# Kernel optimization log

Hardware: AMD Instinct MI355X
Metric: run time of the kernel (lower is better)

The kernel has to match this reference:

```python
import jax, jax.numpy as jnp
import numpy as np

LN_EPS = 1e-3  # keras LayerNormalization default epsilon
LEAKY_SLOPE = 0.2  # tf 'leaky_relu' default alpha


def layer_norm(x, gamma, beta):
    mu = jnp.mean(x, axis=-1, keepdims=True)
    var = jnp.mean(jnp.square(x - mu), axis=-1, keepdims=True)
    return (x - mu) * jax.lax.rsqrt(var + LN_EPS) * gamma + beta


def attention_head(q_in, kv_in, Wk, Wv, Wq, causal):
    # q_in: [b, sq, d], kv_in: [b, sk, d]
    K = jnp.einsum('bsd,de->bse', kv_in, Wk)
    V = jnp.einsum('bsd,de->bse', kv_in, Wv)
    Q = jnp.einsum('bsd,de->bse', q_in, Wq)
    sk = K.shape[1]
    # NOTE: original scales by sqrt(window_size_keys), i.e. key seq length
    scores = jnp.einsum('bqe,bke->bqk', Q, K) / jnp.sqrt(jnp.float32(sk))
    if causal:
        sq = Q.shape[1]
        mask = jnp.triu(jnp.full((sq, sk), -jnp.inf, dtype=scores.dtype), k=1)
        scores = scores + mask
    probs = jax.nn.softmax(scores, axis=-1)
    return jnp.einsum('bqk,bke->bqe', probs, V)


def setup_inputs() -> dict:
    key = jax.random.key(0)
    ks = jax.random.split(key, 12)
    B, S, D, H = 4, 4096, 256, 400
    p = lambda k, shp: jax.random.normal(k, shp, dtype=jnp.float32) * 0.1
    return {
        'inputs': jax.random.normal(ks[0], (B, S, D), dtype=jnp.float32),
        'context_sequence': jax.random.normal(ks[1], (B, S, D), dtype=jnp.float32),
        'sa_Wk': p(ks[2], (D, D)),
        'sa_Wv': p(ks[3], (D, D)),
        'sa_Wq': p(ks[4], (D, D)),
        'ca_Wk': p(ks[5], (D, D)),
        'ca_Wv': p(ks[6], (D, D)),
        'ca_Wq': p(ks[7], (D, D)),
        'W1': p(ks[8], (D, H)),
        'b1': jnp.zeros((H,), dtype=jnp.float32),
        'W2': p(ks[9], (H, D)),
        'b2': jnp.zeros((D,), dtype=jnp.float32),
        'gamma': jnp.ones((D,), dtype=jnp.float32),
        'beta': jnp.zeros((D,), dtype=jnp.float32),
    }


def reference(inputs, context_sequence, sa_Wk, sa_Wv, sa_Wq, ca_Wk, ca_Wv, ca_Wq,
              W1, b1, W2, b2, gamma, beta):
    # 1) masked self-attention + residual + LN (shared LN params)
    in_attn = attention_head(inputs, inputs, sa_Wk, sa_Wv, sa_Wq, causal=True)
    x = layer_norm(in_attn + inputs, gamma, beta)
    # 2) unmasked cross-attention (queries = x, keys/values = context) + residual + LN
    ctx_attn = attention_head(x, context_sequence, ca_Wk, ca_Wv, ca_Wq, causal=False)
    y = layer_norm(ctx_attn + x, gamma, beta)
    # 3) FFN (Dense 400 leaky_relu -> Dense emb) + residual + LN
    h = jax.nn.leaky_relu(jnp.einsum('bsd,dh->bsh', y, W1) + b1, negative_slope=LEAKY_SLOPE)
    ff = jnp.einsum('bsh,hd->bsd', h, W2) + b2
    return layer_norm(ff + y, gamma, beta)
```

## Files before the change

kernel.cpp:

```cpp
#include <hip/hip_runtime.h>

typedef __bf16  bf16x4 __attribute__((ext_vector_type(4)));
typedef __bf16  bf16x8 __attribute__((ext_vector_type(8)));
typedef float   f32x4  __attribute__((ext_vector_type(4)));
typedef unsigned int u32;

constexpr int BM = 128, BN = 128, BK = 32;

__device__ __forceinline__ void async_cp16(const __bf16* g, __bf16* lds) {
    __builtin_amdgcn_global_load_lds(
        (const __attribute__((address_space(1))) u32*)g,
        (__attribute__((address_space(3))) u32*)lds, 16, 0, 0);
}

__device__ __forceinline__ int swz(int row, int q) {
    return row * BK + (((q + (row >> 1)) & 3) << 3);
}

template<int EPI>
__launch_bounds__(256)
__global__ void gemm_nt(const __bf16* __restrict__ Aall, const __bf16* __restrict__ Ball,
                        const float* __restrict__ bias,
                        void* __restrict__ C0, void* __restrict__ C1, void* __restrict__ C2,
                        int N, int K, long ldb, long sA, long sB, long sC,
                        int nTx, int klen, long pstrideB)
{
    const int bx = blockIdx.x;
    const int chunk = bx / nTx;
    const int n0 = (bx - chunk * nTx) * BN;
    const int m0 = blockIdx.y * BM;
    const int bz = blockIdx.z;
    const int kbase = chunk * klen;

    const __bf16* A  = Aall + (long)bz * sA;
    const __bf16* Bt = Ball + (long)bz * sB;

    __shared__ alignas(16) __bf16 As[BM * BK];
    __shared__ alignas(16) __bf16 Bs[BN * BK];

    const int tid = threadIdx.x;
    const int wave = tid >> 6, lane = tid & 63;
    const int wm = (wave >> 1) * 64, wn = (wave & 1) * 64;
    const int quad = lane >> 4, l16 = lane & 15;

    const int row0 = tid >> 2, sl0 = tid & 3;
    const int ks0 = (sl0 - (row0 >> 1)) & 3;
    const int row1 = row0 + 64;
    const int ks1 = (sl0 - (row1 >> 1)) & 3;
    const __bf16* gA0 = A  + (long)(m0 + row0) * K + kbase + ks0 * 8;
    const __bf16* gA1 = A  + (long)(m0 + row1) * K + kbase + ks1 * 8;
    const __bf16* gB0 = Bt + (long)(n0 + row0) * ldb + kbase + ks0 * 8;
    const __bf16* gB1 = Bt + (long)(n0 + row1) * ldb + kbase + ks1 * 8;
    __bf16* ldsA0 = As + wave * 512;
    __bf16* ldsA1 = As + 2048 + wave * 512;
    __bf16* ldsB0 = Bs + wave * 512;
    __bf16* ldsB1 = Bs + 2048 + wave * 512;

    f32x4 acc[4][4];
    #pragma unroll
    for (int i = 0; i < 4; i++)
        #pragma unroll
        for (int j = 0; j < 4; j++) { f32x4 z = {0.f, 0.f, 0.f, 0.f}; acc[i][j] = z; }

    for (int kk = 0; kk < klen; kk += BK) {
        __syncthreads();
        async_cp16(gA0, ldsA0);
        async_cp16(gA1, ldsA1);
        async_cp16(gB0, ldsB0);
        async_cp16(gB1, ldsB1);
        gA0 += BK; gA1 += BK; gB0 += BK; gB1 += BK;
        __syncthreads();

        bf16x8 af[4], bg[4];
        #pragma unroll
        for (int i = 0; i < 4; i++) {
            af[i] = *(const bf16x8*)(As + swz(wm + i * 16 + l16, quad));
            bg[i] = *(const bf16x8*)(Bs + swz(wn + i * 16 + l16, quad));
        }
        #pragma unroll
        for (int i = 0; i < 4; i++)
            #pragma unroll
            for (int j = 0; j < 4; j++)
                acc[i][j] = __builtin_amdgcn_mfma_f32_16x16x32_bf16(af[i], bg[j], acc[i][j], 0, 0, 0);
    }

    char* cb = (char*)C0 + (EPI == 3 ? (long)chunk * pstrideB : 0);
    #pragma unroll
    for (int j = 0; j < 4; j++) {
        const int col = n0 + wn + j * 16 + l16;
        const float bv = (EPI == 2) ? bias[col] : 0.f;
        #pragma unroll
        for (int i = 0; i < 4; i++) {
            #pragma unroll
            for (int r = 0; r < 4; r++) {
                const int row = m0 + wm + i * 16 + quad * 4 + r;
                float c = acc[i][j][r];
                if (EPI == 2) { c += bv; c = c > 0.f ? c : 0.2f * c; }
                if (EPI == 1 || EPI == 3)
                    ((__bf16*)cb)[(long)bz * sC + (long)row * N + col] = (__bf16)c;
                else if (EPI == 2)
                    ((__bf16*)cb)[(long)row * N + col] = (__bf16)c;
                else {
                    const int seg = col >> 8;
                    __bf16* dst = seg == 0 ? (__bf16*)C0 : (seg == 1 ? (__bf16*)C1 : (__bf16*)C2);
                    dst[(long)row * 256 + (col & 255)] = (__bf16)c;
                }
            }
        }
    }
}

template<bool CAUSAL>
__launch_bounds__(256)
__global__ void scores_nt(const __bf16* __restrict__ Qall, const __bf16* __restrict__ Kall,
                          __bf16* __restrict__ SCall, float* __restrict__ side, float scale)
{
    constexpr int S = 4096, KD = 256;
    const int kt = blockIdx.x, mt = blockIdx.y;
    if (CAUSAL && kt > (mt | 1)) return;
    const int n0 = kt * 64, m0 = mt * 64;
    const int bz = blockIdx.z;
    const __bf16* Q  = Qall + (long)bz * S * KD;
    const __bf16* Kp = Kall + (long)bz * S * KD;

    __shared__ alignas(16) __bf16 As[64 * 64];
    __shared__ alignas(16) __bf16 Bs[64 * 64];

    const int tid = threadIdx.x;
    const int wave = tid >> 6, lane = tid & 63;
    const int quad = lane >> 4, l16 = lane & 15;
    const int wq = wave * 16;

    const int rowb = tid >> 3;
    const int gslot = (tid & 7) ^ (rowb & 7);
    const __bf16* gA0 = Q  + (long)(m0 + rowb) * KD + gslot * 8;
    const __bf16* gA1 = Q  + (long)(m0 + 32 + rowb) * KD + gslot * 8;
    const __bf16* gB0 = Kp + (long)(n0 + rowb) * KD + gslot * 8;
    const __bf16* gB1 = Kp + (long)(n0 + 32 + rowb) * KD + gslot * 8;
    const int wb = (tid & ~63) * 8;

    f32x4 acc[4];
    #pragma unroll
    for (int j = 0; j < 4; j++) { f32x4 z = {0.f, 0.f, 0.f, 0.f}; acc[j] = z; }

    for (int kk = 0; kk < KD; kk += 64) {
        __syncthreads();
        async_cp16(gA0 + kk, As + wb);
        async_cp16(gA1 + kk, As + 2048 + wb);
        async_cp16(gB0 + kk, Bs + wb);
        async_cp16(gB1 + kk, Bs + 2048 + wb);
        __syncthreads();
        #pragma unroll
        for (int t2 = 0; t2 < 2; t2++) {
            const int ra = wq + l16;
            bf16x8 af = *(const bf16x8*)(As + ra * 64 + (((t2 * 4 + quad) ^ (ra & 7)) << 3));
            #pragma unroll
            for (int j = 0; j < 4; j++) {
                const int rb = j * 16 + l16;
                bf16x8 bg = *(const bf16x8*)(Bs + rb * 64 + (((t2 * 4 + quad) ^ (rb & 7)) << 3));
                acc[j] = __builtin_amdgcn_mfma_f32_16x16x32_bf16(af, bg, acc[j], 0, 0, 0);
            }
        }
    }

    __bf16* sc = SCall + (long)bz * S * S;
    float se[4] = {0.f, 0.f, 0.f, 0.f};
    #pragma unroll
    for (int j = 0; j < 4; j++) {
        const int col = n0 + j * 16 + l16;
        #pragma unroll
        for (int r = 0; r < 4; r++) {
            const int row = m0 + wq + quad * 4 + r;
            float e = __expf(acc[j][r] * scale);
            if (CAUSAL && kt >= mt && col > row) e = 0.f;
            sc[(long)row * S + col] = (__bf16)e;
            se[r] += e;
        }
    }
    #pragma unroll
    for (int st = 1; st < 16; st <<= 1)
        #pragma unroll
        for (int r = 0; r < 4; r++) se[r] += __shfl_xor(se[r], st);
    if (l16 == 0) {
        float* sd = side + ((long)bz * 64 + kt) * 4096;
        #pragma unroll
        for (int r = 0; r < 4; r++) sd[m0 + wq + quad * 4 + r] = se[r];
    }
}

template<int CMODE>
__launch_bounds__(256)
__global__ void pv_nt(const __bf16* __restrict__ SCall, const __bf16* __restrict__ Vt,
                      __bf16* __restrict__ pbuf, int nsplit, long pstrideE)
{
    constexpr int S = 4096, D = 256, R = 16384;
    const int bx = blockIdx.x;
    const int lin = (bx >> 5) * 8 + (bx & 7);
    const int nt = (bx >> 3) & 3;
    const int per_b = 32 * nsplit;
    const int bz = lin / per_b;
    const int rem = lin - bz * per_b;
    const int chunk = rem >> 5;
    const int m0 = (rem & 31) * 128;
    const int n0 = nt * 64;
    int kbase, klocal;
    if (CMODE == 2) { const int kl = (m0 + 128) / nsplit; kbase = chunk * kl; klocal = kl; }
    else            { const int kl = S / nsplit;          kbase = chunk * kl; klocal = kl; }

    const __bf16* A = SCall + (long)bz * S * S;
    const __bf16* B = Vt + (long)bz * S;

    __shared__ alignas(16) __bf16 As[128 * 32];
    __shared__ alignas(16) __bf16 Bs[64 * 32];

    const int tid = threadIdx.x;
    const int wave = tid >> 6, lane = tid & 63;
    const int wm = (wave >> 1) * 64, wn2 = (wave & 1) * 32;
    const int quad = lane >> 4, l16 = lane & 15;

    const int row0 = tid >> 2, sl0 = tid & 3;
    const int ks0 = (sl0 - (row0 >> 1)) & 3;
    const int row1 = row0 + 64;
    const int ks1 = (sl0 - (row1 >> 1)) & 3;
    const __bf16* gA0 = A + (long)(m0 + row0) * S + kbase + ks0 * 8;
    const __bf16* gA1 = A + (long)(m0 + row1) * S + kbase + ks1 * 8;
    const __bf16* gB0 = B + (long)(n0 + row0) * R + kbase + ks0 * 8;
    __bf16* ldsA0 = As + wave * 512;
    __bf16* ldsA1 = As + 2048 + wave * 512;
    __bf16* ldsB0 = Bs + wave * 512;

    f32x4 acc[4][2];
    #pragma unroll
    for (int i = 0; i < 4; i++)
        #pragma unroll
        for (int j = 0; j < 2; j++) { f32x4 z = {0.f, 0.f, 0.f, 0.f}; acc[i][j] = z; }

    for (int kk = 0; kk < klocal; kk += 32) {
        __syncthreads();
        async_cp16(gA0, ldsA0);
        async_cp16(gA1, ldsA1);
        async_cp16(gB0, ldsB0);
        gA0 += 32; gA1 += 32; gB0 += 32;
        __syncthreads();

        bf16x8 af[4], bg[2];
        #pragma unroll
        for (int i = 0; i < 4; i++)
            af[i] = *(const bf16x8*)(As + swz(wm + i * 16 + l16, quad));
        #pragma unroll
        for (int j = 0; j < 2; j++)
            bg[j] = *(const bf16x8*)(Bs + swz(wn2 + j * 16 + l16, quad));
        #pragma unroll
        for (int i = 0; i < 4; i++)
            #pragma unroll
            for (int j = 0; j < 2; j++)
                acc[i][j] = __builtin_amdgcn_mfma_f32_16x16x32_bf16(af[i], bg[j], acc[i][j], 0, 0, 0);
    }

    __bf16* cb = pbuf + (long)chunk * pstrideE + (long)bz * S * D;
    #pragma unroll
    for (int j = 0; j < 2; j++) {
        const int col = n0 + wn2 + j * 16 + l16;
        #pragma unroll
        for (int i = 0; i < 4; i++)
            #pragma unroll
            for (int r = 0; r < 4; r++) {
                const int row = m0 + wm + i * 16 + quad * 4 + r;
                cb[(long)row * D + col] = (__bf16)acc[i][j][r];
            }
    }
}

template<bool CAUSAL>
__global__ void reduce_inv(const float* __restrict__ side, float* __restrict__ inv)
{
    const int i = blockIdx.x * 256 + threadIdx.x;
    const int b = i >> 12, r = i & 4095;
    const float* sp = side + (long)b * 64 * 4096 + r;
    const int lim = CAUSAL ? 2 * ((r >> 7) + 1) : 64;
    float s = 0.f;
    for (int t = 0; t < lim; t++) s += sp[(long)t * 4096];
    inv[i] = 1.f / s;
}

template<int NP>
__launch_bounds__(256)
__global__ void ln_res(const __bf16* __restrict__ p, long pstr,
                       const float* __restrict__ resid, const float* __restrict__ invs,
                       const float* __restrict__ bias,
                       const float* __restrict__ gamma, const float* __restrict__ beta,
                       float* __restrict__ outf, __bf16* __restrict__ outb)
{
    const int row  = blockIdx.x * 4 + (threadIdx.x >> 6);
    const int lane = threadIdx.x & 63;
    const long vi = (long)row * 64 + lane;
    float p0 = 0.f, p1 = 0.f, p2 = 0.f, p3 = 0.f;
    #pragma unroll
    for (int i = 0; i < NP; i++) {
        bf16x4 vp = ((const bf16x4*)(p + (long)i * pstr))[vi];
        p0 += (float)vp[0]; p1 += (float)vp[1]; p2 += (float)vp[2]; p3 += (float)vp[3];
    }
    if (invs) { const float iv = invs[row]; p0 *= iv; p1 *= iv; p2 *= iv; p3 *= iv; }
    float4 vr = ((const float4*)resid)[vi];
    float x0 = vr.x + p0, x1 = vr.y + p1, x2 = vr.z + p2, x3 = vr.w + p3;
    if (bias) {
        float4 vb = ((const float4*)bias)[lane];
        x0 += vb.x; x1 += vb.y; x2 += vb.z; x3 += vb.w;
    }
    float s = x0 + x1 + x2 + x3;
    #pragma unroll
    for (int off = 32; off; off >>= 1) s += __shfl_xor(s, off);
    const float mu = s * (1.f / 256.f);
    float d0 = x0 - mu, d1 = x1 - mu, d2 = x2 - mu, d3 = x3 - mu;
    float s2 = d0 * d0 + d1 * d1 + d2 * d2 + d3 * d3;
    #pragma unroll
    for (int off = 32; off; off >>= 1) s2 += __shfl_xor(s2, off);
    const float rs = rsqrtf(s2 * (1.f / 256.f) + 1e-3f);
    const float4 g  = ((const float4*)gamma)[lane];
    const float4 be = ((const float4*)beta)[lane];
    float o0 = d0 * rs * g.x + be.x, o1 = d1 * rs * g.y + be.y;
    float o2 = d2 * rs * g.z + be.z, o3 = d3 * rs * g.w + be.w;
    float4 o; o.x = o0; o.y = o1; o.z = o2; o.w = o3;
    ((float4*)outf)[vi] = o;
    if (outb) {
        bf16x4 ob; ob[0] = (__bf16)o0; ob[1] = (__bf16)o1; ob[2] = (__bf16)o2; ob[3] = (__bf16)o3;
        ((bf16x4*)outb)[vi] = ob;
    }
}

__device__ __forceinline__ void tp(const float* __restrict__ src, __bf16* __restrict__ dst,
                                   int rows, int cols, int rowsP, int i)
{
    const int c = i / rowsP, r = i - c * rowsP;
    const float v = (r < rows && c < cols) ? src[r * cols + c] : 0.f;
    dst[i] = (__bf16)v;
}

__global__ void prep_all(const float4* __restrict__ inA, const float4* __restrict__ inC,
                         bf16x4* __restrict__ outA, bf16x4* __restrict__ outC,
                         const float* __restrict__ sWq, const float* __restrict__ sWk,
                         const float* __restrict__ sWv,
                         const float* __restrict__ cWq, const float* __restrict__ cWk,
                         const float* __restrict__ cWv,
                         const float* __restrict__ W1, const float* __restrict__ W2,
                         __bf16* __restrict__ wqk_s, __bf16* __restrict__ wv_s,
                         __bf16* __restrict__ wq_c, __bf16* __restrict__ wk_c,
                         __bf16* __restrict__ wv_c,
                         __bf16* __restrict__ W1t, __bf16* __restrict__ W2t,
                         const float* __restrict__ b1, float* __restrict__ b1p)
{
    const int bx = blockIdx.x, tid = threadIdx.x;
    if (bx < 8192) {
        const bool a = bx < 4096;
        const long j = (long)(a ? bx : bx - 4096) * 256 + tid;
        float4 v = (a ? inA : inC)[j];
        bf16x4 o; o[0] = (__bf16)v.x; o[1] = (__bf16)v.y; o[2] = (__bf16)v.z; o[3] = (__bf16)v.w;
        (a ? outA : outC)[j] = o;
    }
    else if (bx < 8448)  tp(sWq, wqk_s,          256, 256, 256, (bx - 8192)  * 256 + tid);
    else if (bx < 8704)  tp(sWk, wqk_s + 65536,  256, 256, 256, (bx - 8448)  * 256 + tid);
    else if (bx < 8960)  tp(sWv, wv_s,           256, 256, 256, (bx - 8704)  * 256 + tid);
    else if (bx < 9216)  tp(cWq, wq_c,           256, 256, 256, (bx - 8960)  * 256 + tid);
    else if (bx < 9472)  tp(cWk, wk_c,           256, 256, 256, (bx - 9216)  * 256 + tid);
    else if (bx < 9728)  tp(cWv, wv_c,           256, 256, 256, (bx - 9472)  * 256 + tid);
    else if (bx < 10240) tp(W1,  W1t,            256, 400, 256, (bx - 9728)  * 256 + tid);
    else if (bx < 10752) tp(W2,  W2t,            400, 256, 512, (bx - 10240) * 256 + tid);
    else { const int i = (bx - 10752) * 256 + tid; if (i < 512) b1p[i] = (i < 400) ? b1[i] : 0.f; }
}

extern "C" void kernel_launch(void* const* d_in, const int* in_sizes, int n_in,
                              void* d_out, int out_size, void* d_ws, size_t ws_size,
                              hipStream_t stream)
{
    constexpr int B = 4, S = 4096, D = 256, H = 400, Hp = 512;
    constexpr int R = B * S;
    constexpr float SCALE = 1.f / 64.f;

    const float* inputs = (const float*)d_in[0];
    const float* ctx    = (const float*)d_in[1];
    const float* sa_Wk  = (const float*)d_in[2];
    const float* sa_Wv  = (const float*)d_in[3];
    const float* sa_Wq  = (const float*)d_in[4];
    const float* ca_Wk  = (const float*)d_in[5];
    const float* ca_Wv  = (const float*)d_in[6];
    const float* ca_Wq  = (const float*)d_in[7];
    const float* W1     = (const float*)d_in[8];
    const float* b1     = (const float*)d_in[9];
    const float* W2     = (const float*)d_in[10];
    const float* b2     = (const float*)d_in[11];
    const float* gamma  = (const float*)d_in[12];
    const float* beta   = (const float*)d_in[13];
    float* out = (float*)d_out;

    char* ws = (char*)d_ws;
    size_t off = 0;
    auto alloc = [&](size_t bytes) -> char* {
        char* p = ws + off; off += (bytes + 255) & ~size_t(255); return p;
    };
    __bf16* bfA  = (__bf16*)alloc((size_t)R * D * 2);
    __bf16* bfC  = (__bf16*)alloc((size_t)R * D * 2);
    __bf16* Qb   = (__bf16*)alloc((size_t)R * D * 2);
    __bf16* Kb   = (__bf16*)alloc((size_t)R * D * 2);
    __bf16* Vt   = (__bf16*)alloc((size_t)D * R * 2);
    __bf16* h    = (__bf16*)alloc((size_t)R * Hp * 2);
    float*  x    = (float*)alloc((size_t)R * D * 4);
    float*  y    = (float*)alloc((size_t)R * D * 4);
    float*  side = (float*)alloc((size_t)B * 64 * S * 4);
    float*  invb = (float*)alloc((size_t)B * S * 4);
    __bf16* wqk_s = (__bf16*)alloc((size_t)2 * D * D * 2);
    __bf16* wv_s  = (__bf16*)alloc((size_t)D * D * 2);
    __bf16* wq_c  = (__bf16*)alloc((size_t)D * D * 2);
    __bf16* wk_c  = (__bf16*)alloc((size_t)D * D * 2);
    __bf16* wv_c  = (__bf16*)alloc((size_t)D * D * 2);
    __bf16* W1t  = (__bf16*)alloc((size_t)Hp * D * 2);
    __bf16* W2t  = (__bf16*)alloc((size_t)D * Hp * 2);
    float*  b1p  = (float*)alloc((size_t)Hp * 4);

    const size_t PBb = (size_t)R * D * 2;
    const size_t SCB = (size_t)B * S * S * 2;
    size_t rem = ws_size > off ? ws_size - off : 0;
    int NS;
    if      (rem >= 4 * PBb + SCB) NS = 4;
    else if (rem >= 2 * PBb + SCB) NS = 2;
    else if (rem >= 1 * PBb + SCB) NS = 1;
    else return;
    __bf16* pbuf = (__bf16*)alloc((size_t)NS * PBb);
    __bf16* SC   = (__bf16*)(ws + off);
    const long PBe = (long)R * D;

    __bf16* xbf = bfA;
    __bf16* ybf = bfC;

    const dim3 blk(256);
    const int pvGrid = 4 * 32 * NS * B;
    const dim3 gSc(64, 64, B);

    auto launch_ln = [&](int np, const float* res, const float* invs, const float* bias,
                         float* of, __bf16* ob) {
        if (np == 4)      ln_res<4><<<R / 4, blk, 0, stream>>>(pbuf, PBe, res, invs, bias, gamma, beta, of, ob);
        else if (np == 2) ln_res<2><<<R / 4, blk, 0, stream>>>(pbuf, PBe, res, invs, bias, gamma, beta, of, ob);
        else              ln_res<1><<<R / 4, blk, 0, stream>>>(pbuf, PBe, res, invs, bias, gamma, beta, of, ob);
    };

    prep_all<<<10754, blk, 0, stream>>>((const float4*)inputs, (const float4*)ctx,
        (bf16x4*)bfA, (bf16x4*)bfC, sa_Wq, sa_Wk, sa_Wv, ca_Wq, ca_Wk, ca_Wv, W1, W2,
        wqk_s, wv_s, wq_c, wk_c, wv_c, W1t, W2t, b1, b1p);

    gemm_nt<4><<<dim3(4, 128, 1), blk, 0, stream>>>(bfA, wqk_s, nullptr,
        Qb, Kb, nullptr, 2 * D, D, D, 0, 0, 0, 4, D, 0);
    gemm_nt<1><<<dim3(128, 2, 1), blk, 0, stream>>>(wv_s, bfA, nullptr,
        Vt, nullptr, nullptr, R, D, D, 0, 0, 0, 128, D, 0);
    scores_nt<true><<<gSc, blk, 0, stream>>>(Qb, Kb, SC, side, SCALE);
    reduce_inv<true><<<R / 256, blk, 0, stream>>>(side, invb);
    pv_nt<2><<<pvGrid, blk, 0, stream>>>(SC, Vt, pbuf, NS, PBe);
    launch_ln(NS, inputs, invb, nullptr, x, xbf);

    gemm_nt<1><<<dim3(2, 128, 1), blk, 0, stream>>>(xbf, wq_c, nullptr,
        Qb, nullptr, nullptr, D, D, D, 0, 0, 0, 2, D, 0);
    gemm_nt<1><<<dim3(2, 128, 1), blk, 0, stream>>>(bfC, wk_c, nullptr,
        Kb, nullptr, nullptr, D, D, D, 0, 0, 0, 2, D, 0);
    gemm_nt<1><<<dim3(128, 2, 1), blk, 0, stream>>>(wv_c, bfC, nullptr,
        Vt, nullptr, nullptr, R, D, D, 0, 0, 0, 128, D, 0);
    scores_nt<false><<<gSc, blk, 0, stream>>>(Qb, Kb, SC, side, SCALE);
    reduce_inv<false><<<R / 256, blk, 0, stream>>>(side, invb);
    pv_nt<0><<<pvGrid, blk, 0, stream>>>(SC, Vt, pbuf, NS, PBe);
    launch_ln(NS, x, invb, nullptr, y, ybf);

    gemm_nt<2><<<dim3(4, 128, 1), blk, 0, stream>>>(ybf, W1t, b1p,
        h, nullptr, nullptr, Hp, D, D, 0, 0, 0, 4, D, 0);
    gemm_nt<3><<<dim3(2 * NS, 128, 1), blk, 0, stream>>>(h, W2t, nullptr,
        pbuf, nullptr, nullptr, D, Hp, Hp, 0, 0, 0, 2, Hp / NS, (long)PBb);
    launch_ln(NS, y, nullptr, b2, out, nullptr);
}
```

Before: 477.9 us.

## Fuse scores and PV into a flash-style attention kernel with split-K chunks

Replaces the separate scores kernel, which wrote an exp(score) matrix of size B*S*S in bf16 to global memory, and the PV GEMM that read it back, with one fused kernel. The fused kernel computes QK^T per 64-key tile, exponentiates into LDS, and multiplies by V, double-buffering K/V tiles in LDS and splitting the key range across a chunk grid dimension. This removes the large score-matrix round trip and a launch per attention stage. The trade-offs are a large LDS footprint (about 145 KB per block) and a fixed split count, which lowers occupancy. The softmax still has no max subtraction, same as before.

```diff
diff --git a/kernel.cpp b/kernel.cpp
--- a/kernel.cpp
+++ b/kernel.cpp
@@ -110,174 +110,169 @@
     }
 }
 
-template<bool CAUSAL>
-__launch_bounds__(256)
-__global__ void scores_nt(const __bf16* __restrict__ Qall, const __bf16* __restrict__ Kall,
-                          __bf16* __restrict__ SCall, float* __restrict__ side, float scale)
-{
-    constexpr int S = 4096, KD = 256;
-    const int kt = blockIdx.x, mt = blockIdx.y;
-    if (CAUSAL && kt > (mt | 1)) return;
-    const int n0 = kt * 64, m0 = mt * 64;
+template<int CAUSAL>
+__launch_bounds__(512, 2)
+__global__ void fattn(const __bf16* __restrict__ Qall, const __bf16* __restrict__ Kall,
+                      const __bf16* __restrict__ Vt,
+                      __bf16* __restrict__ pbuf, float* __restrict__ side,
+                      int NS, long pstrideE, float scale)
+{
+    constexpr int S = 4096, D = 256, R = 16384;
+    const int mt = CAUSAL ? (int)(gridDim.x - 1 - blockIdx.x) : (int)blockIdx.x;
+    const int chunk = blockIdx.y;
     const int bz = blockIdx.z;
-    const __bf16* Q  = Qall + (long)bz * S * KD;
-    const __bf16* Kp = Kall + (long)bz * S * KD;
-
-    __shared__ alignas(16) __bf16 As[64 * 64];
-    __shared__ alignas(16) __bf16 Bs[64 * 64];
+    const int m0 = mt * 128;
+
+    const int T = CAUSAL ? ((m0 + 128) >> 6) : (S >> 6);
+    const int t0 = chunk * T / NS;
+    const int t1 = (chunk + 1) * T / NS;
+    const int kbase = t0 << 6;
+    const int ntile = t1 - t0;
+
+    const __bf16* Q  = Qall + ((long)bz * S + m0) * D;
+    const __bf16* Kp = Kall + (long)bz * S * D;
+    const long vcol0 = (long)bz * S;
+
+    __shared__ alignas(16) __bf16 Ks[2][16384];
+    __shared__ alignas(16) __bf16 Vs[2][16384];
+    __shared__ alignas(16) __bf16 Ps[128 * 64];
+    __shared__ float sred[8][32];
 
     const int tid = threadIdx.x;
     const int wave = tid >> 6, lane = tid & 63;
     const int quad = lane >> 4, l16 = lane & 15;
-    const int wq = wave * 16;
-
-    const int rowb = tid >> 3;
-    const int gslot = (tid & 7) ^ (rowb & 7);
-    const __bf16* gA0 = Q  + (long)(m0 + rowb) * KD + gslot * 8;
-    const __bf16* gA1 = Q  + (long)(m0 + 32 + rowb) * KD + gslot * 8;
-    const __bf16* gB0 = Kp + (long)(n0 + rowb) * KD + gslot * 8;
-    const __bf16* gB1 = Kp + (long)(n0 + 32 + rowb) * KD + gslot * 8;
-    const int wb = (tid & ~63) * 8;
-
-    f32x4 acc[4];
-    #pragma unroll
-    for (int j = 0; j < 4; j++) { f32x4 z = {0.f, 0.f, 0.f, 0.f}; acc[j] = z; }
-
-    for (int kk = 0; kk < KD; kk += 64) {
+    const int wq32 = (wave >> 1) * 32;
+    const int wk = (wave & 1) * 32;
+    const int we = (wave & 1) * 128;
+
+    bf16x8 qf[2][8];
+    #pragma unroll
+    for (int i = 0; i < 2; i++)
+        #pragma unroll
+        for (int kd = 0; kd < 8; kd++)
+            qf[i][kd] = *(const bf16x8*)(Q + (long)(wq32 + i * 16 + l16) * D + kd * 32 + quad * 8);
+
+    const int srowK = (tid >> 2) & 63;
+    const int srowV = tid >> 2;
+    const int ks8 = (((tid & 3) - (tid >> 3)) & 3) << 3;
+    const int wbase = (tid & ~63) * 8;
+
+    f32x4 acc[2][8];
+    #pragma unroll
+    for (int i = 0; i < 2; i++)
+        #pragma unroll
+        for (int j = 0; j < 8; j++) { f32x4 z = {0.f, 0.f, 0.f, 0.f}; acc[i][j] = z; }
+    float se[2][4] = {{0.f,0.f,0.f,0.f},{0.f,0.f,0.f,0.f}};
+
+    auto stage = [&](int buf, int kb) {
+        const __bf16* gK = Kp + (long)(kb + srowK) * D + ks8 + ((tid >> 8) << 5);
+        #pragma unroll
+        for (int c = 0; c < 4; c++)
+            async_cp16(gK + c * 64, Ks[buf] + c * 4096 + wbase);
+        const __bf16* gV = Vt + vcol0 + kb + ks8;
+        #pragma unroll
+        for (int c = 0; c < 4; c++)
+            async_cp16(gV + (long)(((c & 1) << 7) + srowV) * R + ((c >> 1) << 5),
+                       Vs[buf] + c * 4096 + wbase);
+    };
+
+    if (ntile > 0) stage(0, kbase);
+
+    for (int t = 0; t < ntile; ++t) {
         __syncthreads();
-        async_cp16(gA0 + kk, As + wb);
-        async_cp16(gA1 + kk, As + 2048 + wb);
-        async_cp16(gB0 + kk, Bs + wb);
-        async_cp16(gB1 + kk, Bs + 2048 + wb);
+        const int kb = kbase + (t << 6);
+        if (t + 1 < ntile) stage((t + 1) & 1, kb + 64);
+
+        const __bf16* Kb_ = Ks[t & 1];
+        const __bf16* Vb_ = Vs[t & 1];
+
+        f32x4 sacc[2][2];
+        #pragma unroll
+        for (int i = 0; i < 2; i++)
+            #pragma unroll
+            for (int j = 0; j < 2; j++) { f32x4 z = {0.f, 0.f, 0.f, 0.f}; sacc[i][j] = z; }
+        #pragma unroll
+        for (int kd = 0; kd < 8; kd++) {
+            bf16x8 b0 = *(const bf16x8*)(Kb_ + kd * 2048 + swz(wk + l16, quad));
+            bf16x8 b1 = *(const bf16x8*)(Kb_ + kd * 2048 + swz(wk + 16 + l16, quad));
+            sacc[0][0] = __builtin_amdgcn_mfma_f32_16x16x32_bf16(qf[0][kd], b0, sacc[0][0], 0, 0, 0);
+            sacc[1][0] = __builtin_amdgcn_mfma_f32_16x16x32_bf16(qf[1][kd], b0, sacc[1][0], 0, 0, 0);
+            sacc[0][1] = __builtin_amdgcn_mfma_f32_16x16x32_bf16(qf[0][kd], b1, sacc[0][1], 0, 0, 0);
+            sacc[1][1] = __builtin_amdgcn_mfma_f32_16x16x32_bf16(qf[1][kd], b1, sacc[1][1], 0, 0, 0);
+        }
+
+        const bool diag = CAUSAL && (kb >= m0);
+        #pragma unroll
+        for (int i = 0; i < 2; i++)
+            #pragma unroll
+            for (int j = 0; j < 2; j++) {
+                const int kloc = wk + j * 16 + l16;
+                #pragma unroll
+                for (int r = 0; r < 4; r++) {
+                    const int qloc = wq32 + i * 16 + quad * 4 + r;
+                    float e = __expf(sacc[i][j][r] * scale);
+                    if (diag && kb + kloc > m0 + qloc) e = 0.f;
+                    se[i][r] += e;
+                    Ps[qloc * 64 + (((kloc >> 3) ^ (qloc & 7)) << 3) + (kloc & 7)] = (__bf16)e;
+                }
+            }
         __syncthreads();
-        #pragma unroll
-        for (int t2 = 0; t2 < 2; t2++) {
-            const int ra = wq + l16;
-            bf16x8 af = *(const bf16x8*)(As + ra * 64 + (((t2 * 4 + quad) ^ (ra & 7)) << 3));
-            #pragma unroll
-            for (int j = 0; j < 4; j++) {
-                const int rb = j * 16 + l16;
-                bf16x8 bg = *(const bf16x8*)(Bs + rb * 64 + (((t2 * 4 + quad) ^ (rb & 7)) << 3));
-                acc[j] = __builtin_amdgcn_mfma_f32_16x16x32_bf16(af, bg, acc[j], 0, 0, 0);
+
+        #pragma unroll
+        for (int kc = 0; kc < 2; kc++) {
+            const int sx = (kc * 4 + quad) ^ (l16 & 7);
+            bf16x8 pa0 = *(const bf16x8*)(Ps + (wq32 + l16) * 64 + (sx << 3));
+            bf16x8 pa1 = *(const bf16x8*)(Ps + (wq32 + 16 + l16) * 64 + (sx << 3));
+            #pragma unroll
+            for (int jn = 0; jn < 8; jn++) {
+                bf16x8 vb = *(const bf16x8*)(Vb_ + kc * 8192 + swz(we + jn * 16 + l16, quad));
+                acc[0][jn] = __builtin_amdgcn_mfma_f32_16x16x32_bf16(pa0, vb, acc[0][jn], 0, 0, 0);
+                acc[1][jn] = __builtin_amdgcn_mfma_f32_16x16x32_bf16(pa1, vb, acc[1][jn], 0, 0, 0);
             }
         }
     }
 
-    __bf16* sc = SCall + (long)bz * S * S;
-    float se[4] = {0.f, 0.f, 0.f, 0.f};
-    #pragma unroll
-    for (int j = 0; j < 4; j++) {
-        const int col = n0 + j * 16 + l16;
-        #pragma unroll
-        for (int r = 0; r < 4; r++) {
-            const int row = m0 + wq + quad * 4 + r;
-            float e = __expf(acc[j][r] * scale);
-            if (CAUSAL && kt >= mt && col > row) e = 0.f;
-            sc[(long)row * S + col] = (__bf16)e;
-            se[r] += e;
-        }
-    }
     #pragma unroll
     for (int st = 1; st < 16; st <<= 1)
         #pragma unroll
-        for (int r = 0; r < 4; r++) se[r] += __shfl_xor(se[r], st);
-    if (l16 == 0) {
-        float* sd = side + ((long)bz * 64 + kt) * 4096;
-        #pragma unroll
-        for (int r = 0; r < 4; r++) sd[m0 + wq + quad * 4 + r] = se[r];
-    }
-}
-
-template<int CMODE>
-__launch_bounds__(256)
-__global__ void pv_nt(const __bf16* __restrict__ SCall, const __bf16* __restrict__ Vt,
-                      __bf16* __restrict__ pbuf, int nsplit, long pstrideE)
-{
-    constexpr int S = 4096, D = 256, R = 16384;
-    const int bx = blockIdx.x;
-    const int lin = (bx >> 5) * 8 + (bx & 7);
-    const int nt = (bx >> 3) & 3;
-    const int per_b = 32 * nsplit;
-    const int bz = lin / per_b;
-    const int rem = lin - bz * per_b;
-    const int chunk = rem >> 5;
-    const int m0 = (rem & 31) * 128;
-    const int n0 = nt * 64;
-    int kbase, klocal;
-    if (CMODE == 2) { const int kl = (m0 + 128) / nsplit; kbase = chunk * kl; klocal = kl; }
-    else            { const int kl = S / nsplit;          kbase = chunk * kl; klocal = kl; }
-
-    const __bf16* A = SCall + (long)bz * S * S;
-    const __bf16* B = Vt + (long)bz * S;
-
-    __shared__ alignas(16) __bf16 As[128 * 32];
-    __shared__ alignas(16) __bf16 Bs[64 * 32];
-
-    const int tid = threadIdx.x;
-    const int wave = tid >> 6, lane = tid & 63;
-    const int wm = (wave >> 1) * 64, wn2 = (wave & 1) * 32;
-    const int quad = lane >> 4, l16 = lane & 15;
-
-    const int row0 = tid >> 2, sl0 = tid & 3;
-    const int ks0 = (sl0 - (row0 >> 1)) & 3;
-    const int row1 = row0 + 64;
-    const int ks1 = (sl0 - (row1 >> 1)) & 3;
-    const __bf16* gA0 = A + (long)(m0 + row0) * S + kbase + ks0 * 8;
-    const __bf16* gA1 = A + (long)(m0 + row1) * S + kbase + ks1 * 8;
-    const __bf16* gB0 = B + (long)(n0 + row0) * R + kbase + ks0 * 8;
-    __bf16* ldsA0 = As + wave * 512;
-    __bf16* ldsA1 = As + 2048 + wave * 512;
-    __bf16* ldsB0 = Bs + wave * 512;
-
-    f32x4 acc[4][2];
-    #pragma unroll
-    for (int i = 0; i < 4; i++)
-        #pragma unroll
-        for (int j = 0; j < 2; j++) { f32x4 z = {0.f, 0.f, 0.f, 0.f}; acc[i][j] = z; }
-
-    for (int kk = 0; kk < klocal; kk += 32) {
-        __syncthreads();
-        async_cp16(gA0, ldsA0);
-        async_cp16(gA1, ldsA1);
-        async_cp16(gB0, ldsB0);
-        gA0 += 32; gA1 += 32; gB0 += 32;
-        __syncthreads();
-
-        bf16x8 af[4], bg[2];
-        #pragma unroll
-        for (int i = 0; i < 4; i++)
-            af[i] = *(const bf16x8*)(As + swz(wm + i * 16 + l16, quad));
-        #pragma unroll
-        for (int j = 0; j < 2; j++)
-            bg[j] = *(const bf16x8*)(Bs + swz(wn2 + j * 16 + l16, quad));
-        #pragma unroll
-        for (int i = 0; i < 4; i++)
-            #pragma unroll
-            for (int j = 0; j < 2; j++)
-                acc[i][j] = __builtin_amdgcn_mfma_f32_16x16x32_bf16(af[i], bg[j], acc[i][j], 0, 0, 0);
-    }
-
-    __bf16* cb = pbuf + (long)chunk * pstrideE + (long)bz * S * D;
-    #pragma unroll
-    for (int j = 0; j < 2; j++) {
-        const int col = n0 + wn2 + j * 16 + l16;
-        #pragma unroll
-        for (int i = 0; i < 4; i++)
+        for (int i = 0; i < 2; i++)
+            #pragma unroll
+            for (int r = 0; r < 4; r++) se[i][r] += __shfl_xor(se[i][r], st);
+    if (l16 == 0)
+        #pragma unroll
+        for (int i = 0; i < 2; i++)
+            #pragma unroll
+            for (int r = 0; r < 4; r++)
+                sred[wave][i * 16 + quad * 4 + r] = se[i][r];
+    __syncthreads();
+    if ((wave & 1) == 0 && l16 == 0) {
+        float* sd = side + ((long)bz * 64 + chunk) * 4096 + m0 + wq32;
+        #pragma unroll
+        for (int i = 0; i < 2; i++)
             #pragma unroll
             for (int r = 0; r < 4; r++) {
-                const int row = m0 + wm + i * 16 + quad * 4 + r;
-                cb[(long)row * D + col] = (__bf16)acc[i][j][r];
+                const int idx = i * 16 + quad * 4 + r;
+                sd[idx] = sred[wave][idx] + sred[wave + 1][idx];
             }
     }
-}
-
-template<bool CAUSAL>
-__global__ void reduce_inv(const float* __restrict__ side, float* __restrict__ inv)
+
+    __bf16* cb = pbuf + (long)chunk * pstrideE + ((long)bz * S + m0) * D;
+    #pragma unroll
+    for (int jn = 0; jn < 8; jn++) {
+        const int col = we + jn * 16 + l16;
+        #pragma unroll
+        for (int i = 0; i < 2; i++)
+            #pragma unroll
+            for (int r = 0; r < 4; r++)
+                cb[(long)(wq32 + i * 16 + quad * 4 + r) * D + col] = (__bf16)acc[i][jn][r];
+    }
+}
+
+__global__ void reduce_inv_n(const float* __restrict__ side, float* __restrict__ inv, int lim)
 {
     const int i = blockIdx.x * 256 + threadIdx.x;
     const int b = i >> 12, r = i & 4095;
     const float* sp = side + (long)b * 64 * 4096 + r;
-    const int lim = CAUSAL ? 2 * ((r >> 7) + 1) : 64;
     float s = 0.f;
     for (int t = 0; t < lim; t++) s += sp[(long)t * 4096];
     inv[i] = 1.f / s;
@@ -375,6 +370,9 @@
     constexpr int B = 4, S = 4096, D = 256, H = 400, Hp = 512;
     constexpr int R = B * S;
     constexpr float SCALE = 1.f / 64.f;
+    constexpr int NSc = 4;
+    constexpr int NSx = 2;
+    constexpr int NSf = 2;
 
     const float* inputs = (const float*)d_in[0];
     const float* ctx    = (const float*)d_in[1];
@@ -417,23 +415,15 @@
     float*  b1p  = (float*)alloc((size_t)Hp * 4);
 
     const size_t PBb = (size_t)R * D * 2;
-    const size_t SCB = (size_t)B * S * S * 2;
-    size_t rem = ws_size > off ? ws_size - off : 0;
-    int NS;
-    if      (rem >= 4 * PBb + SCB) NS = 4;
-    else if (rem >= 2 * PBb + SCB) NS = 2;
-    else if (rem >= 1 * PBb + SCB) NS = 1;
-    else return;
-    __bf16* pbuf = (__bf16*)alloc((size_t)NS * PBb);
-    __bf16* SC   = (__bf16*)(ws + off);
+    __bf16* pbuf = (__bf16*)alloc((size_t)4 * PBb);
+    if (off > ws_size) return;
     const long PBe = (long)R * D;
 
     __bf16* xbf = bfA;
     __bf16* ybf = bfC;
 
     const dim3 blk(256);
-    const int pvGrid = 4 * 32 * NS * B;
-    const dim3 gSc(64, 64, B);
+    const dim3 blk512(512);
 
     auto launch_ln = [&](int np, const float* res, const float* invs, const float* bias,
                          float* of, __bf16* ob) {
@@ -450,10 +440,9 @@
         Qb, Kb, nullptr, 2 * D, D, D, 0, 0, 0, 4, D, 0);
     gemm_nt<1><<<dim3(128, 2, 1), blk, 0, stream>>>(wv_s, bfA, nullptr,
         Vt, nullptr, nullptr, R, D, D, 0, 0, 0, 128, D, 0);
-    scores_nt<true><<<gSc, blk, 0, stream>>>(Qb, Kb, SC, side, SCALE);
-    reduce_inv<true><<<R / 256, blk, 0, stream>>>(side, invb);
-    pv_nt<2><<<pvGrid, blk, 0, stream>>>(SC, Vt, pbuf, NS, PBe);
-    launch_ln(NS, inputs, invb, nullptr, x, xbf);
+    fattn<1><<<dim3(32, NSc, B), blk512, 0, stream>>>(Qb, Kb, Vt, pbuf, side, NSc, PBe, SCALE);
+    reduce_inv_n<<<R / 256, blk, 0, stream>>>(side, invb, NSc);
+    launch_ln(NSc, inputs, invb, nullptr, x, xbf);
 
     gemm_nt<1><<<dim3(2, 128, 1), blk, 0, stream>>>(xbf, wq_c, nullptr,
         Qb, nullptr, nullptr, D, D, D, 0, 0, 0, 2, D, 0);
@@ -461,14 +450,13 @@
         Kb, nullptr, nullptr, D, D, D, 0, 0, 0, 2, D, 0);
     gemm_nt<1><<<dim3(128, 2, 1), blk, 0, stream>>>(wv_c, bfC, nullptr,
         Vt, nullptr, nullptr, R, D, D, 0, 0, 0, 128, D, 0);
-    scores_nt<false><<<gSc, blk, 0, stream>>>(Qb, Kb, SC, side, SCALE);
-    reduce_inv<false><<<R / 256, blk, 0, stream>>>(side, invb);
-    pv_nt<0><<<pvGrid, blk, 0, stream>>>(SC, Vt, pbuf, NS, PBe);
-    launch_ln(NS, x, invb, nullptr, y, ybf);
+    fattn<0><<<dim3(32, NSx, B), blk512, 0, stream>>>(Qb, Kb, Vt, pbuf, side, NSx, PBe, SCALE);
+    reduce_inv_n<<<R / 256, blk, 0, stream>>>(side, invb, NSx);
+    launch_ln(NSx, x, invb, nullptr, y, ybf);
 
     gemm_nt<2><<<dim3(4, 128, 1), blk, 0, stream>>>(ybf, W1t, b1p,
         h, nullptr, nullptr, Hp, D, D, 0, 0, 0, 4, D, 0);
-    gemm_nt<3><<<dim3(2 * NS, 128, 1), blk, 0, stream>>>(h, W2t, nullptr,
-        pbuf, nullptr, nullptr, D, Hp, Hp, 0, 0, 0, 2, Hp / NS, (long)PBb);
-    launch_ln(NS, y, nullptr, b2, out, nullptr);
-}
+    gemm_nt<3><<<dim3(2 * NSf, 128, 1), blk, 0, stream>>>(h, W2t, nullptr,
+        pbuf, nullptr, nullptr, D, Hp, Hp, 0, 0, 0, 2, Hp / NSf, (long)PBb);
+    launch_ln(NSf, y, nullptr, b2, out, nullptr);
+}
```

Result: faster. 409.6 us (-14.3%).
